# Kernel tuning notes

Hardware: AMD Instinct MI355X
Metric: run time of the kernel (lower is better)

## Reference

```python
import jax, jax.numpy as jnp
import numpy as np

ALPHA = 0.2  # LeakyReLU negative slope
NEG_BIG = -9e15


def setup_inputs() -> dict:
    key = jax.random.key(0)
    k1, k2, k3, k4 = jax.random.split(key, 4)
    N, F_IN, F_OUT = 8192, 256, 128
    h = jax.random.normal(k1, (N, F_IN), dtype=jnp.float32)
    adj = jax.random.randint(k2, (N, N), 0, 2, dtype=jnp.int32)
    # xavier_uniform with gain=1.414
    def xavier(k, shape, gain=1.414):
        fan_in, fan_out = shape[0], shape[1]
        bound = gain * np.sqrt(6.0 / (fan_in + fan_out))
        return jax.random.uniform(k, shape, jnp.float32, -bound, bound)
    W = xavier(k3, (F_IN, F_OUT))
    a = xavier(k4, (2 * F_OUT, 1))
    return {"h": h, "adj": adj, "W": W, "a": a}


def reference(h, adj, W, a):
    # Wh: [N, F_out]
    Wh = h @ W
    F_out = W.shape[1]
    a1 = a[:F_out, 0]   # attends to source (row) node
    a2 = a[F_out:, 0]   # attends to target (col) node
    # Additive decomposition of concat([Wh_i, Wh_j]) @ a:
    # e[i, j] = leaky_relu(Wh_i . a1 + Wh_j . a2)
    f1 = Wh @ a1  # [N]
    f2 = Wh @ a2  # [N]
    e = jax.nn.leaky_relu(f1[:, None] + f2[None, :], negative_slope=ALPHA)  # [N, N]
    scores = jnp.where(adj > 0, e, jnp.float32(NEG_BIG))
    attention = jax.nn.softmax(scores, axis=1)
    # dropout is identity in eval mode (training=False)
    h_prime = attention @ Wh  # [N, F_out]
    return h_prime
```

## Files before the change

### kernel.cpp

```cpp
#include <hip/hip_runtime.h>


#define N_NODES 8192
#define F_IN 256
#define F_OUT 128
#define RPB 32
#define JCH 128
#define JSPLIT 2
#define JRANGE (N_NODES / JSPLIT)
#define NCH (JRANGE / JCH)

typedef _Float16 half8 __attribute__((ext_vector_type(8)));
typedef float floatx4 __attribute__((ext_vector_type(4)));
typedef float f32x4 __attribute__((ext_vector_type(4)));

__device__ __align__(16) float g_Wh[N_NODES * F_OUT];
__device__ __align__(16) _Float16 g_WhT[(size_t)F_OUT * N_NODES];
__device__ __align__(16) float g_f1[N_NODES];
__device__ __align__(16) float g_f2[N_NODES];
__device__ __align__(16) float g_part[JSPLIT][N_NODES * F_OUT];
__device__ __align__(16) float g_spart[JSPLIT][N_NODES];
__device__ __align__(16) unsigned char g_bits[(size_t)N_NODES * (N_NODES / 8)];

__global__ __launch_bounds__(256) void pack_kernel(const int* __restrict__ adj) {
  const int t = threadIdx.x;
  const int wave = t >> 6;
  const int lane = t & 63;
  const int row0 = blockIdx.x * 8 + wave * 2;
#pragma unroll 1
  for (int rr = 0; rr < 2; ++rr) {
    const int r = row0 + rr;
    const int* rowp = adj + (size_t)r * N_NODES;
#pragma unroll 4
    for (int p = 0; p < 16; ++p) {
      const int j0 = p * 512 + lane * 8;
      const int4 v0 = *(const int4*)(rowp + j0);
      const int4 v1 = *(const int4*)(rowp + j0 + 4);
      unsigned int byte = 0;
      byte |= (v0.x != 0) ? 1u : 0u;
      byte |= (v0.y != 0) ? 2u : 0u;
      byte |= (v0.z != 0) ? 4u : 0u;
      byte |= (v0.w != 0) ? 8u : 0u;
      byte |= (v1.x != 0) ? 16u : 0u;
      byte |= (v1.y != 0) ? 32u : 0u;
      byte |= (v1.z != 0) ? 64u : 0u;
      byte |= (v1.w != 0) ? 128u : 0u;
      const int b = p * 64 + lane;
      const int addr = r * 1024 + (((b >> 2) & 3) * 4 + (b & 3)) * 64 + (b >> 4);
      g_bits[addr] = (unsigned char)byte;
    }
  }
}

__global__ __launch_bounds__(256, 2) void wh_kernel(
    const float* __restrict__ h, const float* __restrict__ W) {
  __shared__ float hT[F_IN][20];
  const int t = threadIdx.x;
  const int i0 = blockIdx.x * 16;
  {
    const int row = t >> 4;
    const int fu = t & 15;
#pragma unroll
    for (int r = 0; r < 4; ++r) {
      const int ku = r * 16 + fu;
      const float4 v = *(const float4*)(h + (size_t)(i0 + row) * F_IN + ku * 4);
      hT[ku * 4 + 0][row] = v.x; hT[ku * 4 + 1][row] = v.y;
      hT[ku * 4 + 2][row] = v.z; hT[ku * 4 + 3][row] = v.w;
    }
  }
  __syncthreads();
  const int c = t & 127;
  const int rg = t >> 7;
  float acc[8];
#pragma unroll
  for (int r = 0; r < 8; ++r) acc[r] = 0.f;
#pragma unroll 8
  for (int k = 0; k < F_IN; ++k) {
    const float wv = W[k * F_OUT + c];
    const float4 x0 = *(const float4*)(&hT[k][rg * 8]);
    const float4 x1 = *(const float4*)(&hT[k][rg * 8 + 4]);
    acc[0] = fmaf(x0.x, wv, acc[0]); acc[1] = fmaf(x0.y, wv, acc[1]);
    acc[2] = fmaf(x0.z, wv, acc[2]); acc[3] = fmaf(x0.w, wv, acc[3]);
    acc[4] = fmaf(x1.x, wv, acc[4]); acc[5] = fmaf(x1.y, wv, acc[5]);
    acc[6] = fmaf(x1.z, wv, acc[6]); acc[7] = fmaf(x1.w, wv, acc[7]);
  }
#pragma unroll
  for (int r = 0; r < 8; ++r)
    g_Wh[(size_t)(i0 + rg * 8 + r) * F_OUT + c] = acc[r];
  union { _Float16 hh[8]; uint4 u4; } pk;
#pragma unroll
  for (int r = 0; r < 8; ++r) pk.hh[r] = (_Float16)acc[r];
  *(uint4*)(g_WhT + (size_t)c * N_NODES + i0 + rg * 8) = pk.u4;
}

__global__ __launch_bounds__(256) void f12_kernel(const float* __restrict__ a) {
  const int t = threadIdx.x;
  const int row = blockIdx.x * 2 + (t >> 7);
  const int c = t & 127;
  const float wh = g_Wh[(size_t)row * F_OUT + c];
  float p1 = wh * a[c];
  float p2 = wh * a[F_OUT + c];
  for (int o = 32; o > 0; o >>= 1) {
    p1 += __shfl_down(p1, o, 64);
    p2 += __shfl_down(p2, o, 64);
  }
  __shared__ float s1[4], s2[4];
  const int w = t >> 6;
  if ((t & 63) == 0) { s1[w] = p1; s2[w] = p2; }
  __syncthreads();
  if ((t & 127) == 0) {
    g_f1[row] = s1[w] + s1[w + 1];
    g_f2[row] = s2[w] + s2[w + 1];
  }
}

__device__ __forceinline__ float score_b(unsigned int bit, float f2v, float f1r) {
  float s = f1r + f2v;
  s = fmaxf(s, 0.2f * s);
  float arg = bit ? fmaf(s, 1.44269504088896f, -16.0f) : -1.0e5f;
  return __builtin_amdgcn_exp2f(arg);
}

__global__ __launch_bounds__(256, 3) void gat_attn_kernel() {
  const int t = threadIdx.x;
  const int wave = t >> 6;
  const int lane = t & 63;
  const int mrow = lane & 15;
  const int quad = lane >> 4;
  const int i0 = blockIdx.x * RPB;
  const int js = blockIdx.y;
  const int jbase = js * JRANGE;

  __shared__ float ldsF2[JRANGE];
  __shared__ float ldsO[RPB][F_OUT];
  __shared__ float ldsS[4][RPB];

  int rm[4], cm[4];
  {
    half8 a1f, b1f, a2f, b2f;
#pragma unroll
    for (int e = 0; e < 8; ++e) {
      a1f[e] = (_Float16)0; b1f[e] = (_Float16)0;
      a2f[e] = (_Float16)0; b2f[e] = (_Float16)0;
    }
    if (quad == 0) {
      a1f[0] = (_Float16)mrow; b1f[0] = (_Float16)1;
      a2f[0] = (_Float16)1;    b2f[0] = (_Float16)mrow;
    }
    floatx4 d1 = (floatx4)0.f, d2 = (floatx4)0.f;
    d1 = __builtin_amdgcn_mfma_f32_16x16x32_f16(a1f, b1f, d1, 0, 0, 0);
    d2 = __builtin_amdgcn_mfma_f32_16x16x32_f16(a2f, b2f, d2, 0, 0, 0);
#pragma unroll
    for (int r = 0; r < 4; ++r) { rm[r] = (int)d1[r]; cm[r] = (int)d2[r]; }
  }

  const float f1r0 = g_f1[i0 + mrow];
  const float f1r1 = g_f1[i0 + 16 + mrow];

  half8 ones;
#pragma unroll
  for (int e = 0; e < 8; ++e) ones[e] = (_Float16)1;

  floatx4 acc[2][8];
  floatx4 asum[2];
#pragma unroll
  for (int tl = 0; tl < 2; ++tl) {
    asum[tl] = (floatx4)0.f;
#pragma unroll
    for (int ct = 0; ct < 8; ++ct) acc[tl][ct] = (floatx4)0.f;
  }

#pragma unroll
  for (int it = 0; it < 4; ++it) {
    const int u = it * 256 + t;
    *(float4*)&ldsF2[u * 4] = *(const float4*)(g_f2 + jbase + u * 4);
  }
  __syncthreads();

  const int wq = wave * 4 + quad;
  const int jloc = wave * 32 + quad * 8;
  const unsigned char* bp0 = g_bits + (i0 + mrow) * 1024 + wq * 64 + js * 32;
  const unsigned char* bp1 = g_bits + (i0 + 16 + mrow) * 1024 + wq * 64 + js * 32;

#pragma unroll 1
  for (int c4 = 0; c4 < NCH / 4; ++c4) {
    const unsigned int dw0 = *(const unsigned int*)(bp0 + c4 * 4);
    const unsigned int dw1 = *(const unsigned int*)(bp1 + c4 * 4);
#pragma unroll
    for (int k = 0; k < 4; ++k) {
      const int c = c4 * 4 + k;
      const int jglob = jbase + c * JCH + jloc;

      half8 bfr[8];
#pragma unroll
      for (int ct = 0; ct < 8; ++ct)
        bfr[ct] = *(const half8*)(g_WhT + (size_t)(ct * 16 + mrow) * N_NODES + jglob);

      const float4 F0 = *(const float4*)&ldsF2[c * JCH + jloc];
      const float4 F1 = *(const float4*)&ldsF2[c * JCH + jloc + 4];

      const unsigned int b0 = (dw0 >> (8 * k)) & 0xffu;
      const unsigned int b1 = (dw1 >> (8 * k)) & 0xffu;

      half8 af0, af1;
      af0[0] = (_Float16)score_b(b0 & 1u,   F0.x, f1r0);
      af0[1] = (_Float16)score_b(b0 & 2u,   F0.y, f1r0);
      af0[2] = (_Float16)score_b(b0 & 4u,   F0.z, f1r0);
      af0[3] = (_Float16)score_b(b0 & 8u,   F0.w, f1r0);
      af0[4] = (_Float16)score_b(b0 & 16u,  F1.x, f1r0);
      af0[5] = (_Float16)score_b(b0 & 32u,  F1.y, f1r0);
      af0[6] = (_Float16)score_b(b0 & 64u,  F1.z, f1r0);
      af0[7] = (_Float16)score_b(b0 & 128u, F1.w, f1r0);
      af1[0] = (_Float16)score_b(b1 & 1u,   F0.x, f1r1);
      af1[1] = (_Float16)score_b(b1 & 2u,   F0.y, f1r1);
      af1[2] = (_Float16)score_b(b1 & 4u,   F0.z, f1r1);
      af1[3] = (_Float16)score_b(b1 & 8u,   F0.w, f1r1);
      af1[4] = (_Float16)score_b(b1 & 16u,  F1.x, f1r1);
      af1[5] = (_Float16)score_b(b1 & 32u,  F1.y, f1r1);
      af1[6] = (_Float16)score_b(b1 & 64u,  F1.z, f1r1);
      af1[7] = (_Float16)score_b(b1 & 128u, F1.w, f1r1);

#pragma unroll
      for (int ct = 0; ct < 8; ++ct) {
        acc[0][ct] = __builtin_amdgcn_mfma_f32_16x16x32_f16(af0, bfr[ct], acc[0][ct], 0, 0, 0);
        acc[1][ct] = __builtin_amdgcn_mfma_f32_16x16x32_f16(af1, bfr[ct], acc[1][ct], 0, 0, 0);
      }
      asum[0] = __builtin_amdgcn_mfma_f32_16x16x32_f16(af0, ones, asum[0], 0, 0, 0);
      asum[1] = __builtin_amdgcn_mfma_f32_16x16x32_f16(af1, ones, asum[1], 0, 0, 0);
    }
  }

  if (mrow == 0) {
#pragma unroll
    for (int tl = 0; tl < 2; ++tl)
#pragma unroll
      for (int r = 0; r < 4; ++r)
        ldsS[wave][tl * 16 + rm[r]] = asum[tl][r];
  }
  for (int w = 0; w < 4; ++w) {
    if (wave == w) {
#pragma unroll
      for (int tl = 0; tl < 2; ++tl)
#pragma unroll
        for (int ct = 0; ct < 8; ++ct)
#pragma unroll
          for (int r = 0; r < 4; ++r) {
            float* p = &ldsO[tl * 16 + rm[r]][ct * 16 + cm[r]];
            if (w == 0) *p = acc[tl][ct][r];
            else        *p += acc[tl][ct][r];
          }
    }
    __syncthreads();
  }
  {
    const int row = t >> 3;
    const int c0 = (t & 7) * 16;
    float* dst = g_part[js] + (size_t)(i0 + row) * F_OUT + c0;
#pragma unroll
    for (int q = 0; q < 4; ++q)
      *(f32x4*)(dst + q * 4) = *(const f32x4*)(&ldsO[row][c0 + q * 4]);
    if (t < RPB)
      g_spart[js][i0 + t] = ldsS[0][t] + ldsS[1][t] + ldsS[2][t] + ldsS[3][t];
  }
}

__global__ __launch_bounds__(256) void comb_kernel(float* __restrict__ out) {
  const int u = blockIdx.x * 256 + threadIdx.x;
  const int row = u >> 5;
  const float s = g_spart[0][row] + g_spart[1][row];
  const f32x4 v = ((const f32x4*)g_part[0])[u] + ((const f32x4*)g_part[1])[u];
  ((f32x4*)out)[u] = v * (1.0f / s);
}

extern "C" void kernel_launch(void* const* d_in, const int* in_sizes, int n_in,
                              void* d_out, int out_size, void* d_ws, size_t ws_size,
                              hipStream_t stream) {
  const float* h = (const float*)d_in[0];
  const int* adj = (const int*)d_in[1];
  const float* W = (const float*)d_in[2];
  const float* a = (const float*)d_in[3];
  float* out = (float*)d_out;
  (void)d_ws; (void)ws_size;

  pack_kernel<<<dim3(N_NODES / 8), dim3(256), 0, stream>>>(adj);
  wh_kernel<<<dim3(N_NODES / 16), dim3(256), 0, stream>>>(h, W);
  f12_kernel<<<dim3(N_NODES / 2), dim3(256), 0, stream>>>(a);
  gat_attn_kernel<<<dim3(N_NODES / RPB, JSPLIT), dim3(256), 0, stream>>>();
  comb_kernel<<<dim3(N_NODES * F_OUT / 4 / 256), dim3(256), 0, stream>>>(out);
}
```

Before: 472.1 us.

## Fuse prep kernels, split attention over four column ranges, add nontemporal accesses

Merges adjacency bit-packing, the Wh GEMM and the f1/f2 projection into one prep kernel, with f1/f2 computed from the GEMM accumulators through wave shuffles. This removes two launches and the re-read of Wh. The attention kernel now splits columns four ways over a flattened grid with launch bounds of 2, which doubles the partial buffers the combine kernel must read. Nontemporal loads and stores are added for the streaming data to limit cache pollution.

```diff
diff --git a/kernel.cpp b/kernel.cpp
--- a/kernel.cpp
+++ b/kernel.cpp
@@ -6,13 +6,14 @@
 #define F_OUT 128
 #define RPB 32
 #define JCH 128
-#define JSPLIT 2
+#define JSPLIT 4
 #define JRANGE (N_NODES / JSPLIT)
 #define NCH (JRANGE / JCH)
 
 typedef _Float16 half8 __attribute__((ext_vector_type(8)));
 typedef float floatx4 __attribute__((ext_vector_type(4)));
 typedef float f32x4 __attribute__((ext_vector_type(4)));
+typedef int intx4 __attribute__((ext_vector_type(4)));
 
 __device__ __align__(16) float g_Wh[N_NODES * F_OUT];
 __device__ __align__(16) _Float16 g_WhT[(size_t)F_OUT * N_NODES];
@@ -22,48 +23,53 @@
 __device__ __align__(16) float g_spart[JSPLIT][N_NODES];
 __device__ __align__(16) unsigned char g_bits[(size_t)N_NODES * (N_NODES / 8)];
 
-__global__ __launch_bounds__(256) void pack_kernel(const int* __restrict__ adj) {
+__global__ __launch_bounds__(256, 2) void prep_kernel(
+    const int* __restrict__ adj, const float* __restrict__ h,
+    const float* __restrict__ W, const float* __restrict__ a) {
   const int t = threadIdx.x;
-  const int wave = t >> 6;
-  const int lane = t & 63;
-  const int row0 = blockIdx.x * 8 + wave * 2;
+  const int bid = blockIdx.x;
+
+  if (bid < N_NODES / 8) {
+    const int wave = t >> 6;
+    const int lane = t & 63;
+    const int row0 = bid * 8 + wave * 2;
 #pragma unroll 1
-  for (int rr = 0; rr < 2; ++rr) {
-    const int r = row0 + rr;
-    const int* rowp = adj + (size_t)r * N_NODES;
+    for (int rr = 0; rr < 2; ++rr) {
+      const int r = row0 + rr;
+      const int* rowp = adj + (size_t)r * N_NODES;
 #pragma unroll 4
-    for (int p = 0; p < 16; ++p) {
-      const int j0 = p * 512 + lane * 8;
-      const int4 v0 = *(const int4*)(rowp + j0);
-      const int4 v1 = *(const int4*)(rowp + j0 + 4);
-      unsigned int byte = 0;
-      byte |= (v0.x != 0) ? 1u : 0u;
-      byte |= (v0.y != 0) ? 2u : 0u;
-      byte |= (v0.z != 0) ? 4u : 0u;
-      byte |= (v0.w != 0) ? 8u : 0u;
-      byte |= (v1.x != 0) ? 16u : 0u;
-      byte |= (v1.y != 0) ? 32u : 0u;
-      byte |= (v1.z != 0) ? 64u : 0u;
-      byte |= (v1.w != 0) ? 128u : 0u;
-      const int b = p * 64 + lane;
-      const int addr = r * 1024 + (((b >> 2) & 3) * 4 + (b & 3)) * 64 + (b >> 4);
-      g_bits[addr] = (unsigned char)byte;
-    }
-  }
-}
-
-__global__ __launch_bounds__(256, 2) void wh_kernel(
-    const float* __restrict__ h, const float* __restrict__ W) {
+      for (int p = 0; p < 16; ++p) {
+        const int j0 = p * 512 + lane * 8;
+        const intx4 v0 = __builtin_nontemporal_load((const intx4*)(rowp + j0));
+        const intx4 v1 = __builtin_nontemporal_load((const intx4*)(rowp + j0 + 4));
+        unsigned int byte = 0;
+        byte |= (v0.x != 0) ? 1u : 0u;
+        byte |= (v0.y != 0) ? 2u : 0u;
+        byte |= (v0.z != 0) ? 4u : 0u;
+        byte |= (v0.w != 0) ? 8u : 0u;
+        byte |= (v1.x != 0) ? 16u : 0u;
+        byte |= (v1.y != 0) ? 32u : 0u;
+        byte |= (v1.z != 0) ? 64u : 0u;
+        byte |= (v1.w != 0) ? 128u : 0u;
+        const int b = p * 64 + lane;
+        const int addr = r * 1024 + (((b >> 2) & 3) * 4 + (b & 3)) * 64 + (b >> 4);
+        g_bits[addr] = (unsigned char)byte;
+      }
+    }
+    return;
+  }
+
   __shared__ float hT[F_IN][20];
-  const int t = threadIdx.x;
-  const int i0 = blockIdx.x * 16;
+  __shared__ float fs[2][2][8][2];
+  const int i0 = (bid - N_NODES / 8) * 16;
   {
     const int row = t >> 4;
     const int fu = t & 15;
 #pragma unroll
     for (int r = 0; r < 4; ++r) {
       const int ku = r * 16 + fu;
-      const float4 v = *(const float4*)(h + (size_t)(i0 + row) * F_IN + ku * 4);
+      const f32x4 v = __builtin_nontemporal_load(
+          (const f32x4*)(h + (size_t)(i0 + row) * F_IN + ku * 4));
       hT[ku * 4 + 0][row] = v.x; hT[ku * 4 + 1][row] = v.y;
       hT[ku * 4 + 2][row] = v.z; hT[ku * 4 + 3][row] = v.w;
     }
@@ -91,26 +97,33 @@
 #pragma unroll
   for (int r = 0; r < 8; ++r) pk.hh[r] = (_Float16)acc[r];
   *(uint4*)(g_WhT + (size_t)c * N_NODES + i0 + rg * 8) = pk.u4;
-}
-
-__global__ __launch_bounds__(256) void f12_kernel(const float* __restrict__ a) {
-  const int t = threadIdx.x;
-  const int row = blockIdx.x * 2 + (t >> 7);
-  const int c = t & 127;
-  const float wh = g_Wh[(size_t)row * F_OUT + c];
-  float p1 = wh * a[c];
-  float p2 = wh * a[F_OUT + c];
-  for (int o = 32; o > 0; o >>= 1) {
-    p1 += __shfl_down(p1, o, 64);
-    p2 += __shfl_down(p2, o, 64);
-  }
-  __shared__ float s1[4], s2[4];
-  const int w = t >> 6;
-  if ((t & 63) == 0) { s1[w] = p1; s2[w] = p2; }
+
+  const float a1c = a[c];
+  const float a2c = a[F_OUT + c];
+  float p1[8], p2[8];
+#pragma unroll
+  for (int r = 0; r < 8; ++r) { p1[r] = acc[r] * a1c; p2[r] = acc[r] * a2c; }
+#pragma unroll
+  for (int o = 32; o > 0; o >>= 1)
+#pragma unroll
+    for (int r = 0; r < 8; ++r) {
+      p1[r] += __shfl_down(p1[r], o, 64);
+      p2[r] += __shfl_down(p2[r], o, 64);
+    }
+  const int wv = t >> 6;
+  const int lane = t & 63;
+  if (lane == 0) {
+#pragma unroll
+    for (int r = 0; r < 8; ++r) {
+      fs[wv >> 1][wv & 1][r][0] = p1[r];
+      fs[wv >> 1][wv & 1][r][1] = p2[r];
+    }
+  }
   __syncthreads();
-  if ((t & 127) == 0) {
-    g_f1[row] = s1[w] + s1[w + 1];
-    g_f2[row] = s2[w] + s2[w + 1];
+  if (t < 16) {
+    const int rg2 = t >> 3, r2 = t & 7;
+    g_f1[i0 + rg2 * 8 + r2] = fs[rg2][0][r2][0] + fs[rg2][1][r2][0];
+    g_f2[i0 + rg2 * 8 + r2] = fs[rg2][0][r2][1] + fs[rg2][1][r2][1];
   }
 }
 
@@ -121,14 +134,15 @@
   return __builtin_amdgcn_exp2f(arg);
 }
 
-__global__ __launch_bounds__(256, 3) void gat_attn_kernel() {
+__global__ __launch_bounds__(256, 2) void gat_attn_kernel() {
   const int t = threadIdx.x;
   const int wave = t >> 6;
   const int lane = t & 63;
   const int mrow = lane & 15;
   const int quad = lane >> 4;
-  const int i0 = blockIdx.x * RPB;
-  const int js = blockIdx.y;
+  const int flat = blockIdx.x;
+  const int js = flat & 3;
+  const int i0 = (flat >> 2) * RPB;
   const int jbase = js * JRANGE;
 
   __shared__ float ldsF2[JRANGE];
@@ -171,7 +185,7 @@
   }
 
 #pragma unroll
-  for (int it = 0; it < 4; ++it) {
+  for (int it = 0; it < 2; ++it) {
     const int u = it * 256 + t;
     *(float4*)&ldsF2[u * 4] = *(const float4*)(g_f2 + jbase + u * 4);
   }
@@ -179,13 +193,15 @@
 
   const int wq = wave * 4 + quad;
   const int jloc = wave * 32 + quad * 8;
-  const unsigned char* bp0 = g_bits + (i0 + mrow) * 1024 + wq * 64 + js * 32;
-  const unsigned char* bp1 = g_bits + (i0 + 16 + mrow) * 1024 + wq * 64 + js * 32;
+  const unsigned char* bp0 = g_bits + (i0 + mrow) * 1024 + wq * 64 + js * (JRANGE / 128);
+  const unsigned char* bp1 = g_bits + (i0 + 16 + mrow) * 1024 + wq * 64 + js * (JRANGE / 128);
 
 #pragma unroll 1
   for (int c4 = 0; c4 < NCH / 4; ++c4) {
-    const unsigned int dw0 = *(const unsigned int*)(bp0 + c4 * 4);
-    const unsigned int dw1 = *(const unsigned int*)(bp1 + c4 * 4);
+    const unsigned int dw0 =
+        __builtin_nontemporal_load((const unsigned int*)(bp0 + c4 * 4));
+    const unsigned int dw1 =
+        __builtin_nontemporal_load((const unsigned int*)(bp1 + c4 * 4));
 #pragma unroll
     for (int k = 0; k < 4; ++k) {
       const int c = c4 * 4 + k;
@@ -258,7 +274,8 @@
     float* dst = g_part[js] + (size_t)(i0 + row) * F_OUT + c0;
 #pragma unroll
     for (int q = 0; q < 4; ++q)
-      *(f32x4*)(dst + q * 4) = *(const f32x4*)(&ldsO[row][c0 + q * 4]);
+      __builtin_nontemporal_store(*(const f32x4*)(&ldsO[row][c0 + q * 4]),
+                                  (f32x4*)(dst + q * 4));
     if (t < RPB)
       g_spart[js][i0 + t] = ldsS[0][t] + ldsS[1][t] + ldsS[2][t] + ldsS[3][t];
   }
@@ -267,9 +284,13 @@
 __global__ __launch_bounds__(256) void comb_kernel(float* __restrict__ out) {
   const int u = blockIdx.x * 256 + threadIdx.x;
   const int row = u >> 5;
-  const float s = g_spart[0][row] + g_spart[1][row];
-  const f32x4 v = ((const f32x4*)g_part[0])[u] + ((const f32x4*)g_part[1])[u];
-  ((f32x4*)out)[u] = v * (1.0f / s);
+  const float s = g_spart[0][row] + g_spart[1][row] +
+                  g_spart[2][row] + g_spart[3][row];
+  const f32x4 v = __builtin_nontemporal_load(((const f32x4*)g_part[0]) + u) +
+                  __builtin_nontemporal_load(((const f32x4*)g_part[1]) + u) +
+                  __builtin_nontemporal_load(((const f32x4*)g_part[2]) + u) +
+                  __builtin_nontemporal_load(((const f32x4*)g_part[3]) + u);
+  __builtin_nontemporal_store(v * (1.0f / s), ((f32x4*)out) + u);
 }
 
 extern "C" void kernel_launch(void* const* d_in, const int* in_sizes, int n_in,
@@ -282,9 +303,7 @@
   float* out = (float*)d_out;
   (void)d_ws; (void)ws_size;
 
-  pack_kernel<<<dim3(N_NODES / 8), dim3(256), 0, stream>>>(adj);
-  wh_kernel<<<dim3(N_NODES / 16), dim3(256), 0, stream>>>(h, W);
-  f12_kernel<<<dim3(N_NODES / 2), dim3(256), 0, stream>>>(a);
-  gat_attn_kernel<<<dim3(N_NODES / RPB, JSPLIT), dim3(256), 0, stream>>>();
+  prep_kernel<<<dim3(N_NODES / 8 + N_NODES / 16), dim3(256), 0, stream>>>(adj, h, W, a);
+  gat_attn_kernel<<<dim3((N_NODES / RPB) * JSPLIT), dim3(256), 0, stream>>>();
   comb_kernel<<<dim3(N_NODES * F_OUT / 4 / 256), dim3(256), 0, stream>>>(out);
 }
```

After: 470.3 us. No clear change (-0.4%).
